# Performance work log

Hardware: AMD Instinct MI355X
Metric: run time of the kernel (lower is better)

Reference implementation:

```python
import jax, jax.numpy as jnp
import numpy as np

N = 100000      # nodes
E = 1600000     # directed edges (avg degree 16)
F_IN = 128      # in_channels
H = 128         # hidden
G = 64          # graphs in batch


def setup_inputs() -> dict:
    key = jax.random.key(0)
    ks = jax.random.split(key, 9)
    x = jax.random.normal(ks[0], (N, F_IN), dtype=jnp.float32)
    edge_index = jax.random.randint(ks[1], (2, E), 0, N, dtype=jnp.int32)
    batch = jnp.sort(jax.random.randint(ks[2], (N,), 0, G, dtype=jnp.int32))
    # GCNConv weights (glorot-ish scale) and biases
    W1 = jax.random.normal(ks[3], (F_IN, H), dtype=jnp.float32) / np.sqrt(F_IN)
    b1 = jnp.zeros((H,), dtype=jnp.float32)
    W2 = jax.random.normal(ks[4], (H, H // 2), dtype=jnp.float32) / np.sqrt(H)
    b2 = jnp.zeros((H // 2,), dtype=jnp.float32)
    lin_w = jax.random.normal(ks[5], (H // 2, 1), dtype=jnp.float32) / np.sqrt(H // 2)
    lin_b = jnp.zeros((1,), dtype=jnp.float32)
    return {"x": x, "edge_index": edge_index, "batch": batch,
            "W1": W1, "b1": b1, "W2": W2, "b2": b2,
            "lin_w": lin_w, "lin_b": lin_b}


def reference(x, edge_index, batch, W1, b1, W2, b2, lin_w, lin_b):
    n = x.shape[0]
    # GCN default: add self-loops, symmetric deg^-1/2 normalization
    loop = jnp.arange(n, dtype=edge_index.dtype)
    src = jnp.concatenate([edge_index[0], loop])
    dst = jnp.concatenate([edge_index[1], loop])
    deg = jax.ops.segment_sum(jnp.ones_like(dst, dtype=x.dtype), dst, num_segments=n)
    dis = jax.lax.rsqrt(jnp.maximum(deg, 1.0))  # deg >= 1 due to self-loops
    norm = dis[src] * dis[dst]                  # [E+N]

    def gcn_conv(h, W, b):
        h = h @ W                               # transform first (smaller dim on edges)
        m = h[src] * norm[:, None]              # gather + scale  [E+N, d]
        return jax.ops.segment_sum(m, dst, num_segments=n) + b  # scatter-add

    h = jax.nn.relu(gcn_conv(x, W1, b1))        # dropout = identity in eval mode
    h = jax.nn.relu(gcn_conv(h, W2, b2))

    # global_mean_pool over graph ids
    sums = jax.ops.segment_sum(h, batch, num_segments=G)            # [G, H//2]
    cnt = jax.ops.segment_sum(jnp.ones((n,), h.dtype), batch, num_segments=G)
    pooled = sums / jnp.maximum(cnt, 1.0)[:, None]

    return (pooled @ lin_w + lin_b)[:, 0]       # squeeze(-1) -> [G]
```

## Files before the change

### kernel.cpp

```cpp
#include <hip/hip_runtime.h>
#include <hip/hip_fp16.h>


#define DN 512
#define DSHIFT 9

typedef _Float16 half8 __attribute__((ext_vector_type(8)));
typedef float f32x4 __attribute__((ext_vector_type(4)));

__global__ void k_init(int* __restrict__ bucket_cnt, float* __restrict__ psum,
                       float* __restrict__ pcnt, int NBK, int psumN, int G) {
  int i = blockIdx.x * 256 + threadIdx.x;
  if (i < NBK) bucket_cnt[i] = 0;
  if (i < psumN) psum[i] = 0.f;
  if (i < G) pcnt[i] = 0.f;
}

__global__ __launch_bounds__(1024) void k_hist(const int* __restrict__ dst,
                                               int* __restrict__ bucket_cnt,
                                               int E, int NBK) {
  __shared__ int h[256];
  int t = threadIdx.x;
  if (t < 256) h[t] = 0;
  __syncthreads();
  int base = blockIdx.x * 4096;
#pragma unroll
  for (int j = 0; j < 4; ++j) {
    int i = base + j * 1024 + t;
    if (i < E) atomicAdd(&h[dst[i] >> DSHIFT], 1);
  }
  __syncthreads();
  if (t < NBK && h[t] > 0) atomicAdd(&bucket_cnt[t], h[t]);
}

__global__ __launch_bounds__(256) void k_bscan(const int* __restrict__ bucket_cnt,
                                               int* __restrict__ bucket_start,
                                               int* __restrict__ bucket_cursor,
                                               int NBK) {
  __shared__ int sh[256];
  int t = threadIdx.x;
  sh[t] = (t < NBK) ? bucket_cnt[t] : 0;
  __syncthreads();
  for (int off = 1; off < 256; off <<= 1) {
    int v = (t >= off) ? sh[t - off] : 0;
    __syncthreads();
    sh[t] += v;
    __syncthreads();
  }
  if (t < NBK) {
    int st = (t == 0) ? 0 : sh[t - 1];
    bucket_start[t] = st;
    bucket_cursor[t] = st;
  }
}

__global__ __launch_bounds__(1024) void k_split(const int* __restrict__ src,
                                                const int* __restrict__ dst,
                                                int* __restrict__ bucket_cursor,
                                                int2* __restrict__ binned,
                                                int E, int NBK) {
  __shared__ int h[256];
  __shared__ int lcur[256];
  int t = threadIdx.x;
  if (t < 256) h[t] = 0;
  __syncthreads();
  int base = blockIdx.x * 4096;
  int s[4], d[4], b[4];
  bool val[4];
#pragma unroll
  for (int j = 0; j < 4; ++j) {
    int i = base + j * 1024 + t;
    val[j] = (i < E);
    if (val[j]) {
      s[j] = src[i];
      d[j] = dst[i];
      b[j] = d[j] >> DSHIFT;
      atomicAdd(&h[b[j]], 1);
    }
  }
  __syncthreads();
  if (t < NBK && h[t] > 0) lcur[t] = atomicAdd(&bucket_cursor[t], h[t]);
  __syncthreads();
#pragma unroll
  for (int j = 0; j < 4; ++j) {
    if (val[j]) {
      int pos = atomicAdd(&lcur[b[j]], 1);
      binned[pos] = make_int2(s[j], d[j]);
    }
  }
}

__global__ __launch_bounds__(1024) void k_bucket(const int2* __restrict__ binned,
                                                 const int* __restrict__ bucket_start,
                                                 const int* __restrict__ bucket_cnt,
                                                 int* __restrict__ rowptr,
                                                 int* __restrict__ rowend,
                                                 float* __restrict__ dis,
                                                 int* __restrict__ esrc, int N) {
  __shared__ int lcnt[DN];
  __shared__ int lscan[DN];
  int k = blockIdx.x;
  int t = threadIdx.x;
  int bstart = bucket_start[k];
  int cntk = bucket_cnt[k];
  int nbase = k << DSHIFT;
  if (t < DN) lcnt[t] = 0;
  __syncthreads();
  for (int i = t; i < cntk; i += 1024)
    atomicAdd(&lcnt[binned[bstart + i].y - nbase], 1);
  __syncthreads();
  if (t < DN) lscan[t] = lcnt[t];
  __syncthreads();
  for (int off = 1; off < DN; off <<= 1) {
    int v = (t < DN && t >= off) ? lscan[t - off] : 0;
    __syncthreads();
    if (t < DN) lscan[t] += v;
    __syncthreads();
  }
  if (t < DN) {
    int g = nbase + t;
    if (g < N) {
      int inc = lscan[t];
      int c = lcnt[t];
      rowptr[g] = bstart + inc - c;
      rowend[g] = bstart + inc;
      dis[g] = rsqrtf((float)(c + 1));
    }
    lcnt[t] = lscan[t] - lcnt[t];
  }
  __syncthreads();
  for (int i = t; i < cntk; i += 1024) {
    int2 e = binned[bstart + i];
    int slot = atomicAdd(&lcnt[e.y - nbase], 1);
    esrc[bstart + slot] = e.x;
  }
}

template <int COLS, int K>
__global__ __launch_bounds__(256) void k_gemm(const float* __restrict__ A,
                                              const float* __restrict__ W,
                                              const float* __restrict__ dis,
                                              __half* __restrict__ out, int nrows) {
  constexpr int KP = K + 8;
  __shared__ _Float16 As[64 * KP];
  __shared__ _Float16 Wt[64 * KP];
  int t = threadIdx.x;
  int row0 = blockIdx.x * 64;
  int cbase = blockIdx.y * 64;

  {
    int c4 = (t & 15) * 4;
    for (int k = t >> 4; k < K; k += 16) {
      float4 wv = *(const float4*)&W[(size_t)k * COLS + cbase + c4];
      Wt[(c4 + 0) * KP + k] = (_Float16)wv.x;
      Wt[(c4 + 1) * KP + k] = (_Float16)wv.y;
      Wt[(c4 + 2) * KP + k] = (_Float16)wv.z;
      Wt[(c4 + 3) * KP + k] = (_Float16)wv.w;
    }
  }
  {
    constexpr int F4 = K / 4;
    for (int id = t; id < 64 * F4; id += 256) {
      int r = id / F4, kq = (id % F4) * 4;
      int grow = row0 + r;
      float4 av = (grow < nrows) ? *(const float4*)&A[(size_t)grow * K + kq]
                                 : make_float4(0.f, 0.f, 0.f, 0.f);
      _Float16* dst = &As[r * KP + kq];
      dst[0] = (_Float16)av.x;
      dst[1] = (_Float16)av.y;
      dst[2] = (_Float16)av.z;
      dst[3] = (_Float16)av.w;
    }
  }
  __syncthreads();

  int wave = t >> 6, lane = t & 63;
  int m = lane & 15;
  int quad = lane >> 4;

  f32x4 acc[4];
#pragma unroll
  for (int ct = 0; ct < 4; ++ct) acc[ct] = (f32x4){0.f, 0.f, 0.f, 0.f};

  const _Float16* arow = &As[(wave * 16 + m) * KP + quad * 8];
#pragma unroll
  for (int ks = 0; ks < K; ks += 32) {
    half8 af = *(const half8*)&arow[ks];
#pragma unroll
    for (int ct = 0; ct < 4; ++ct) {
      half8 bf = *(const half8*)&Wt[(ct * 16 + m) * KP + quad * 8 + ks];
      acc[ct] = __builtin_amdgcn_mfma_f32_16x16x32_f16(af, bf, acc[ct], 0, 0, 0);
    }
  }

#pragma unroll
  for (int j = 0; j < 4; ++j) {
    int gr = row0 + wave * 16 + quad * 4 + j;
    if (gr < nrows) {
      float dn = dis[gr];
#pragma unroll
      for (int ct = 0; ct < 4; ++ct)
        out[(size_t)gr * COLS + cbase + ct * 16 + m] =
            __float2half_rn(acc[ct][j] * dn);
    }
  }
}

template <int COLS>
__global__ __launch_bounds__(256) void k_agg(const __half* __restrict__ H,
                                             const int* __restrict__ rowptr,
                                             const int* __restrict__ rowend,
                                             const int* __restrict__ esrc,
                                             const float* __restrict__ dis,
                                             const float* __restrict__ bias,
                                             float* __restrict__ out, int n) {
  constexpr int LPE = COLS / 8;
  constexpr int NG = 64 / LPE;
  int node = (blockIdx.x * 256 + threadIdx.x) >> 6;
  if (node >= n) return;
  int lane = threadIdx.x & 63;
  int group = lane / LPE;
  int c = (lane % LPE) * 8;

  float acc[8];
#pragma unroll
  for (int j = 0; j < 8; ++j) acc[j] = 0.f;

  int beg = rowptr[node], end = rowend[node];
  int e0 = beg + group;
  int e1 = e0 + NG;
  int s0 = 0, s1 = 0;
  float w0 = 0.f, w1 = 0.f;
  if (e0 < end) { s0 = esrc[e0]; w0 = 1.f; }
  if (e1 < end) { s1 = esrc[e1]; w1 = 1.f; }
  while (e0 < end) {
    float4 r0 = *(const float4*)&H[(size_t)s0 * COLS + c];
    float4 r1 = *(const float4*)&H[(size_t)s1 * COLS + c];
    int e2 = e0 + 2 * NG, e3 = e1 + 2 * NG;
    int s2 = 0, s3 = 0;
    float w2 = 0.f, w3 = 0.f;
    if (e2 < end) { s2 = esrc[e2]; w2 = 1.f; }
    if (e3 < end) { s3 = esrc[e3]; w3 = 1.f; }
    {
      union { float4 f4; __half2 h2[4]; } u;
      u.f4 = r0;
#pragma unroll
      for (int j = 0; j < 4; ++j) {
        float2 f = __half22float2(u.h2[j]);
        acc[2 * j + 0] = fmaf(f.x, w0, acc[2 * j + 0]);
        acc[2 * j + 1] = fmaf(f.y, w0, acc[2 * j + 1]);
      }
      u.f4 = r1;
#pragma unroll
      for (int j = 0; j < 4; ++j) {
        float2 f = __half22float2(u.h2[j]);
        acc[2 * j + 0] = fmaf(f.x, w1, acc[2 * j + 0]);
        acc[2 * j + 1] = fmaf(f.y, w1, acc[2 * j + 1]);
      }
    }
    e0 = e2; s0 = s2; w0 = w2;
    e1 = e3; s1 = s3; w1 = w3;
  }
#pragma unroll
  for (int m = LPE; m < 64; m <<= 1) {
#pragma unroll
    for (int j = 0; j < 8; ++j) acc[j] += __shfl_xor(acc[j], m, 64);
  }
  if (group == 0) {
    float dn = dis[node];
    union { float4 f4; __half2 h2[4]; } u;
    u.f4 = *(const float4*)&H[(size_t)node * COLS + c];
    float o[8];
#pragma unroll
    for (int j = 0; j < 4; ++j) {
      float2 f = __half22float2(u.h2[j]);
      o[2 * j + 0] = fmaxf(fmaf(acc[2 * j + 0] + f.x, dn, bias[c + 2 * j + 0]), 0.f);
      o[2 * j + 1] = fmaxf(fmaf(acc[2 * j + 1] + f.y, dn, bias[c + 2 * j + 1]), 0.f);
    }
    *(float4*)&out[(size_t)node * COLS + c] = make_float4(o[0], o[1], o[2], o[3]);
    *(float4*)&out[(size_t)node * COLS + c + 4] = make_float4(o[4], o[5], o[6], o[7]);
  }
}

__global__ void k_pool(const float* __restrict__ H2, const int* __restrict__ batch,
                       float* __restrict__ psum, float* __restrict__ pcnt, int n) {
  int wv = (blockIdx.x * 256 + threadIdx.x) >> 6;
  int lane = threadIdx.x & 63;
  int start = wv * 32;
  if (start >= n) return;
  int end = min(start + 32, n);
  int curg = batch[start];
  float acc = 0.f;
  int cn = 0;
  for (int i = start; i < end; ++i) {
    int g = batch[i];
    if (g != curg) {
      atomicAdd(&psum[curg * 64 + lane], acc);
      if (lane == 0) atomicAdd(&pcnt[curg], (float)cn);
      acc = 0.f;
      cn = 0;
      curg = g;
    }
    acc += H2[(size_t)i * 64 + lane];
    ++cn;
  }
  atomicAdd(&psum[curg * 64 + lane], acc);
  if (lane == 0) atomicAdd(&pcnt[curg], (float)cn);
}

__global__ void k_final(const float* __restrict__ psum, const float* __restrict__ pcnt,
                        const float* __restrict__ lin_w, const float* __restrict__ lin_b,
                        float* __restrict__ out, int G) {
  int g = blockIdx.x * 64 + threadIdx.x;
  if (g >= G) return;
  float c = fmaxf(pcnt[g], 1.f);
  float s = 0.f;
  for (int i = 0; i < 64; ++i) s += psum[g * 64 + i] * lin_w[i];
  out[g] = s / c + lin_b[0];
}

extern "C" void kernel_launch(void* const* d_in, const int* in_sizes, int n_in,
                              void* d_out, int out_size, void* d_ws, size_t ws_size,
                              hipStream_t stream) {
  const float* x = (const float*)d_in[0];
  const int* edge = (const int*)d_in[1];
  const int* batch = (const int*)d_in[2];
  const float* W1 = (const float*)d_in[3];
  const float* b1 = (const float*)d_in[4];
  const float* W2 = (const float*)d_in[5];
  const float* b2 = (const float*)d_in[6];
  const float* lin_w = (const float*)d_in[7];
  const float* lin_b = (const float*)d_in[8];
  float* out = (float*)d_out;

  const int N = in_sizes[2];
  const int E = in_sizes[1] / 2;
  const int G = out_size;
  const int* esrc_in = edge;
  const int* edst_in = edge + E;

  char* w = (char*)d_ws;
  size_t off = 0;
  auto take = [&](size_t bytes) {
    void* p = w + off;
    off += (bytes + 255) & ~(size_t)255;
    return p;
  };
  int* bucket_cnt = (int*)take(256 * 4);
  int* bucket_start = (int*)take(256 * 4);
  int* bucket_cursor = (int*)take(256 * 4);
  int* rowptr = (int*)take((size_t)N * 4);
  int* rowend = (int*)take((size_t)N * 4);
  float* dis = (float*)take((size_t)N * 4);
  int* esrc = (int*)take((size_t)E * 4);
  __half* XW = (__half*)take((size_t)N * 128 * 2);
  float* H1 = (float*)take((size_t)N * 128 * 4);
  float* psum = (float*)take((size_t)G * 64 * 4);
  float* pcnt = (float*)take((size_t)G * 4);
  int2* binned = (int2*)XW;
  (void)ws_size;
  (void)n_in;

  const int NBK = (N + DN - 1) / DN;
  const int PB = (E + 4095) / 4096;
  int ib = (max(G * 64, NBK) + 255) / 256;

  k_init<<<ib, 256, 0, stream>>>(bucket_cnt, psum, pcnt, NBK, G * 64, G);
  k_hist<<<PB, 1024, 0, stream>>>(edst_in, bucket_cnt, E, NBK);
  k_bscan<<<1, 256, 0, stream>>>(bucket_cnt, bucket_start, bucket_cursor, NBK);
  k_split<<<PB, 1024, 0, stream>>>(esrc_in, edst_in, bucket_cursor, binned, E, NBK);
  k_bucket<<<NBK, 1024, 0, stream>>>(binned, bucket_start, bucket_cnt,
                                     rowptr, rowend, dis, esrc, N);

  int gb = (N + 63) / 64;
  int ab = (int)(((size_t)N * 64 + 255) / 256);

  k_gemm<128, 128><<<dim3(gb, 2), 256, 0, stream>>>(x, W1, dis, XW, N);
  k_agg<128><<<ab, 256, 0, stream>>>(XW, rowptr, rowend, esrc, dis, b1, H1, N);

  k_gemm<64, 128><<<dim3(gb, 1), 256, 0, stream>>>(H1, W2, dis, XW, N);
  k_agg<64><<<ab, 256, 0, stream>>>(XW, rowptr, rowend, esrc, dis, b2, H1, N);

  int pb = (int)((((size_t)(N + 31) / 32) * 64 + 255) / 256);
  k_pool<<<pb, 256, 0, stream>>>(H1, batch, psum, pcnt, N);
  k_final<<<1, 64, 0, stream>>>(psum, pcnt, lin_w, lin_b, out, G);
}
```

Baseline: 332.9 us.

## Pack binned edges into one int and store hidden activations in fp16

Binned edges are packed into a single 32-bit word (source shifted left plus the destination's offset within its bucket) instead of an int2, halving the scatter and read traffic of the CSR build. The aggregation outputs are now written as fp16 rather than fp32, so the second GEMM loads half8 directly without conversion and pooling reads half the bytes. The packing relies on src << 9 fitting in 32 bits, which holds for N=100000, and fp16 storage of the hidden activations adds rounding error.

```diff
diff --git a/kernel.cpp b/kernel.cpp
--- a/kernel.cpp
+++ b/kernel.cpp
@@ -57,7 +57,7 @@
 __global__ __launch_bounds__(1024) void k_split(const int* __restrict__ src,
                                                 const int* __restrict__ dst,
                                                 int* __restrict__ bucket_cursor,
-                                                int2* __restrict__ binned,
+                                                int* __restrict__ binned,
                                                 int E, int NBK) {
   __shared__ int h[256];
   __shared__ int lcur[256];
@@ -65,16 +65,16 @@
   if (t < 256) h[t] = 0;
   __syncthreads();
   int base = blockIdx.x * 4096;
-  int s[4], d[4], b[4];
+  int pk[4], b[4];
   bool val[4];
 #pragma unroll
   for (int j = 0; j < 4; ++j) {
     int i = base + j * 1024 + t;
     val[j] = (i < E);
     if (val[j]) {
-      s[j] = src[i];
-      d[j] = dst[i];
-      b[j] = d[j] >> DSHIFT;
+      int s = src[i], d = dst[i];
+      b[j] = d >> DSHIFT;
+      pk[j] = (s << DSHIFT) | (d & (DN - 1));
       atomicAdd(&h[b[j]], 1);
     }
   }
@@ -85,12 +85,12 @@
   for (int j = 0; j < 4; ++j) {
     if (val[j]) {
       int pos = atomicAdd(&lcur[b[j]], 1);
-      binned[pos] = make_int2(s[j], d[j]);
-    }
-  }
-}
-
-__global__ __launch_bounds__(1024) void k_bucket(const int2* __restrict__ binned,
+      binned[pos] = pk[j];
+    }
+  }
+}
+
+__global__ __launch_bounds__(1024) void k_bucket(const int* __restrict__ binned,
                                                  const int* __restrict__ bucket_start,
                                                  const int* __restrict__ bucket_cnt,
                                                  int* __restrict__ rowptr,
@@ -107,7 +107,7 @@
   if (t < DN) lcnt[t] = 0;
   __syncthreads();
   for (int i = t; i < cntk; i += 1024)
-    atomicAdd(&lcnt[binned[bstart + i].y - nbase], 1);
+    atomicAdd(&lcnt[binned[bstart + i] & (DN - 1)], 1);
   __syncthreads();
   if (t < DN) lscan[t] = lcnt[t];
   __syncthreads();
@@ -130,14 +130,14 @@
   }
   __syncthreads();
   for (int i = t; i < cntk; i += 1024) {
-    int2 e = binned[bstart + i];
-    int slot = atomicAdd(&lcnt[e.y - nbase], 1);
-    esrc[bstart + slot] = e.x;
-  }
-}
-
-template <int COLS, int K>
-__global__ __launch_bounds__(256) void k_gemm(const float* __restrict__ A,
+    int p = binned[bstart + i];
+    int slot = atomicAdd(&lcnt[p & (DN - 1)], 1);
+    esrc[bstart + slot] = (unsigned)p >> DSHIFT;
+  }
+}
+
+template <int COLS, int K, typename AT>
+__global__ __launch_bounds__(256) void k_gemm(const AT* __restrict__ A,
                                               const float* __restrict__ W,
                                               const float* __restrict__ dis,
                                               __half* __restrict__ out, int nrows) {
@@ -158,7 +158,7 @@
       Wt[(c4 + 3) * KP + k] = (_Float16)wv.w;
     }
   }
-  {
+  if constexpr (sizeof(AT) == 4) {
     constexpr int F4 = K / 4;
     for (int id = t; id < 64 * F4; id += 256) {
       int r = id / F4, kq = (id % F4) * 4;
@@ -171,6 +171,16 @@
       dst[2] = (_Float16)av.z;
       dst[3] = (_Float16)av.w;
     }
+  } else {
+    constexpr int H8 = K / 8;
+    for (int id = t; id < 64 * H8; id += 256) {
+      int r = id / H8, kq = (id % H8) * 8;
+      int grow = row0 + r;
+      half8 av = (grow < nrows)
+                     ? *(const half8*)&A[(size_t)grow * K + kq]
+                     : (half8){0, 0, 0, 0, 0, 0, 0, 0};
+      *(half8*)&As[r * KP + kq] = av;
+    }
   }
   __syncthreads();
 
@@ -213,7 +223,7 @@
                                              const int* __restrict__ esrc,
                                              const float* __restrict__ dis,
                                              const float* __restrict__ bias,
-                                             float* __restrict__ out, int n) {
+                                             __half* __restrict__ out, int n) {
   constexpr int LPE = COLS / 8;
   constexpr int NG = 64 / LPE;
   int node = (blockIdx.x * 256 + threadIdx.x) >> 6;
@@ -270,19 +280,19 @@
     float dn = dis[node];
     union { float4 f4; __half2 h2[4]; } u;
     u.f4 = *(const float4*)&H[(size_t)node * COLS + c];
-    float o[8];
+    union { __half2 h2[4]; float4 f4; } o;
 #pragma unroll
     for (int j = 0; j < 4; ++j) {
       float2 f = __half22float2(u.h2[j]);
-      o[2 * j + 0] = fmaxf(fmaf(acc[2 * j + 0] + f.x, dn, bias[c + 2 * j + 0]), 0.f);
-      o[2 * j + 1] = fmaxf(fmaf(acc[2 * j + 1] + f.y, dn, bias[c + 2 * j + 1]), 0.f);
-    }
-    *(float4*)&out[(size_t)node * COLS + c] = make_float4(o[0], o[1], o[2], o[3]);
-    *(float4*)&out[(size_t)node * COLS + c + 4] = make_float4(o[4], o[5], o[6], o[7]);
-  }
-}
-
-__global__ void k_pool(const float* __restrict__ H2, const int* __restrict__ batch,
+      float ox = fmaxf(fmaf(acc[2 * j + 0] + f.x, dn, bias[c + 2 * j + 0]), 0.f);
+      float oy = fmaxf(fmaf(acc[2 * j + 1] + f.y, dn, bias[c + 2 * j + 1]), 0.f);
+      o.h2[j] = __floats2half2_rn(ox, oy);
+    }
+    *(float4*)&out[(size_t)node * COLS + c] = o.f4;
+  }
+}
+
+__global__ void k_pool(const __half* __restrict__ H2, const int* __restrict__ batch,
                        float* __restrict__ psum, float* __restrict__ pcnt, int n) {
   int wv = (blockIdx.x * 256 + threadIdx.x) >> 6;
   int lane = threadIdx.x & 63;
@@ -301,7 +311,7 @@
       cn = 0;
       curg = g;
     }
-    acc += H2[(size_t)i * 64 + lane];
+    acc += __half2float(H2[(size_t)i * 64 + lane]);
     ++cn;
   }
   atomicAdd(&psum[curg * 64 + lane], acc);
@@ -354,10 +364,10 @@
   float* dis = (float*)take((size_t)N * 4);
   int* esrc = (int*)take((size_t)E * 4);
   __half* XW = (__half*)take((size_t)N * 128 * 2);
-  float* H1 = (float*)take((size_t)N * 128 * 4);
+  __half* H = (__half*)take((size_t)N * 128 * 2);
   float* psum = (float*)take((size_t)G * 64 * 4);
   float* pcnt = (float*)take((size_t)G * 4);
-  int2* binned = (int2*)XW;
+  int* binned = (int*)XW;
   (void)ws_size;
   (void)n_in;
 
@@ -375,13 +385,14 @@
   int gb = (N + 63) / 64;
   int ab = (int)(((size_t)N * 64 + 255) / 256);
 
-  k_gemm<128, 128><<<dim3(gb, 2), 256, 0, stream>>>(x, W1, dis, XW, N);
-  k_agg<128><<<ab, 256, 0, stream>>>(XW, rowptr, rowend, esrc, dis, b1, H1, N);
-
-  k_gemm<64, 128><<<dim3(gb, 1), 256, 0, stream>>>(H1, W2, dis, XW, N);
-  k_agg<64><<<ab, 256, 0, stream>>>(XW, rowptr, rowend, esrc, dis, b2, H1, N);
+  k_gemm<128, 128, float><<<dim3(gb, 2), 256, 0, stream>>>(x, W1, dis, XW, N);
+  k_agg<128><<<ab, 256, 0, stream>>>(XW, rowptr, rowend, esrc, dis, b1, H, N);
+
+  k_gemm<64, 128, _Float16><<<dim3(gb, 1), 256, 0, stream>>>(
+      (const _Float16*)H, W2, dis, XW, N);
+  k_agg<64><<<ab, 256, 0, stream>>>(XW, rowptr, rowend, esrc, dis, b2, H, N);
 
   int pb = (int)((((size_t)(N + 31) / 32) * 64 + 255) / 256);
-  k_pool<<<pb, 256, 0, stream>>>(H1, batch, psum, pcnt, N);
+  k_pool<<<pb, 256, 0, stream>>>(H, batch, psum, pcnt, N);
   k_final<<<1, 64, 0, stream>>>(psum, pcnt, lin_w, lin_b, out, G);
 }
```

Result: faster. 317.0 us (-4.8%).
